# Optimization experiments

Measured on AMD Instinct MI355X. Metric: run time of the kernel, lower is better.

The kernel has to match this reference:

```python
import jax, jax.numpy as jnp
import numpy as np

B, L, D, DEPTH, FF, VOCAB = 2, 2048, 1024, 4, 4096, 32000

def setup_inputs():
    key = jax.random.key(0)
    ks = jax.random.split(key, 16)
    n = lambda k, s, sc: jax.random.normal(k, s, dtype=jnp.float32) * sc
    sw = 0.01 / float(np.sqrt(D))  # xavier_normal with gain 0.01 on square dims
    return dict(
        tokens=jax.random.randint(ks[0], (B, L), 0, VOCAB),
        emb=n(ks[1], (VOCAB, D), 0.02),
        Wz=n(ks[2], (DEPTH, D, D), sw), bz=jnp.zeros((DEPTH, D)),
        Wza=n(ks[3], (DEPTH, D, D), sw), bza=jnp.zeros((DEPTH, D)),
        Wy=n(ks[4], (DEPTH, D, D), sw), by=jnp.zeros((DEPTH, D)),
        Wya=n(ks[5], (DEPTH, D, D), sw), bya=jnp.zeros((DEPTH, D)),
        lc_re=n(ks[6], (DEPTH, D), 1.0), lc_im=n(ks[7], (DEPTH, D), 1.0),
        g_in=jnp.ones((DEPTH, D)), g_sc=jnp.ones((DEPTH, D)), g_ffn=jnp.ones((DEPTH, D)),
        Wf=n(ks[8], (DEPTH, D, FF), 0.02), bf=jnp.zeros((DEPTH, FF)),
        Wfa=n(ks[9], (DEPTH, D, FF), 0.02), bfa=jnp.zeros((DEPTH, FF)),
        Wfo=n(ks[10], (DEPTH, FF, D), 0.02), bfo=jnp.zeros((DEPTH, D)),
        ln_w=jnp.ones((D,)), ln_b=jnp.zeros((D,)),
        Wout=n(ks[11], (D, VOCAB), 0.02), bout=jnp.zeros((VOCAB,)),
    )

def _silu(x):
    return x * jax.nn.sigmoid(x)

def _rms(x, w, eps=1e-6):
    return x * jax.lax.rsqrt(jnp.mean(x * x, axis=-1, keepdims=True) + eps) * w

def reference(tokens, emb, Wz, bz, Wza, bza, Wy, by, Wya, bya, lc_re, lc_im,
              g_in, g_sc, g_ffn, Wf, bf, Wfa, bfa, Wfo, bfo, ln_w, ln_b, Wout, bout):
    Bq, Lq = tokens.shape
    # Embedding with max_norm=1: torch renorms accessed rows to norm <= 1
    e = emb[tokens]
    nrm = jnp.linalg.norm(e, axis=-1, keepdims=True)
    x = e * jnp.minimum(1.0, 1.0 / jnp.maximum(nrm, 1e-7))
    # Decaying phazor kernel (shared across layers; phazor_angle_scale is a fixed buffer)
    angle = jnp.power(0.001, jnp.linspace(0.0, 1.0, D))
    ln_ph = (1e-5 + 1j * angle).astype(jnp.complex64)      # [D]
    t = jnp.arange(Lq, dtype=jnp.float32)
    ph = jnp.exp(t[:, None] * ln_ph[None, :])              # [L, D] complex
    pf = jnp.fft.fft(ph, n=2 * Lq, axis=0)                 # [2L, D]
    decay = jnp.exp(ln_ph)                                 # [D]
    for i in range(DEPTH):
        # --- SConv sublayer (pre-RMSNorm + residual) ---
        xr = x
        xn = _rms(x, g_sc[i])
        z = (xn @ Wz[i] + bz[i]) * _silu(xn @ Wza[i] + bza[i])
        zf = jnp.fft.fft(z.astype(jnp.complex64), n=2 * Lq, axis=1)
        h = jnp.fft.ifft(zf * pf[None], axis=1)[:, :Lq]    # inner-chunk causal decaying conv
        lc = (lc_re[i] + 1j * lc_im[i]).astype(jnp.complex64)
        h = h + lc[None, None, :] * ph[None] * decay[None, None, :]  # cross-chunk state carry
        y = (_rms(h.real, g_in[i]) @ Wy[i] + by[i]) * _silu(xn @ Wya[i] + bya[i])
        x = xr + y
        # --- FFN SwiGLU sublayer (pre-RMSNorm + residual) ---
        xr = x
        xn = _rms(x, g_ffn[i])
        x = xr + ((xn @ Wf[i] + bf[i]) * _silu(xn @ Wfa[i] + bfa[i])) @ Wfo[i] + bfo[i]
    # Final LayerNorm + vocab projection
    mu = jnp.mean(x, axis=-1, keepdims=True)
    var = jnp.mean((x - mu) ** 2, axis=-1, keepdims=True)
    x = (x - mu) * jax.lax.rsqrt(var + 1e-5) * ln_w + ln_b
    return x @ Wout + bout
```

## Files before the change

kernel.cpp:

```cpp
#include <hip/hip_runtime.h>
#include <math.h>

typedef __attribute__((ext_vector_type(8))) short bf16x8;
typedef __attribute__((ext_vector_type(4))) float f32x4;

#define DEVI __device__ __forceinline__

DEVI short f2bf(float f) {
  unsigned u = __builtin_bit_cast(unsigned, f);
  return (short)((u + 0x7fffu + ((u >> 16) & 1u)) >> 16);
}
DEVI float bf2f(short s) {
  unsigned u = ((unsigned)(unsigned short)s) << 16;
  return __builtin_bit_cast(float, u);
}

DEVI float silu_f(float v) { return v / (1.0f + expf(-v)); }

DEVI void async16(const void* g, void* l) {
  __builtin_amdgcn_global_load_lds(
      (const __attribute__((address_space(1))) void*)g,
      (__attribute__((address_space(3))) void*)l, 16, 0, 0);
}

template <int N>
DEVI void waitvm() { asm volatile("s_waitcnt vmcnt(%0)" ::"i"(N) : "memory"); }
DEVI void barrier_mem() { asm volatile("s_barrier" ::: "memory"); }
DEVI void lgkm0_sb() {
  asm volatile("s_waitcnt lgkmcnt(0)" ::: "memory");
  __builtin_amdgcn_sched_barrier(0);
}

template <int NROWT>
DEVI void tile_map(int* bx, int* by) {
  const int nwg = gridDim.x;
  const int lin = blockIdx.x;
  const int q = nwg >> 3;
  const int wgid = (lin & 7) * q + (lin >> 3);
  *by = wgid % NROWT;
  *bx = wgid / NROWT;
}

#define SWZ(r) ((ks ^ (((r) >> 1) & 3)) << 4)

__global__ __launch_bounds__(512, 1) void gemm8_k(const short* __restrict__ A,
                                                  const short* __restrict__ BT,
                                                  const float* __restrict__ bias,
                                                  float* __restrict__ outp,
                                                  int N, int K) {
  __shared__ __align__(16) char lds[4 * 32768];
  int bx, by;
  tile_map<16>(&bx, &by);
  const int row0 = by << 8, col0 = bx << 8;
  const int t = threadIdx.x, w = t >> 6, lane = t & 63;
  const int wm = w >> 2, wn = w & 3;
  const int lr = lane & 15, ks = lane >> 4;
  f32x4 acc[8][4] = {};

  const int sslot = (t & 3) ^ ((t >> 3) & 3);
  const char* gA = (const char*)A + ((size_t)(row0 + (t >> 2)) * K) * 2 + sslot * 16;
  const char* gB = (const char*)BT + ((size_t)(col0 + (t >> 2)) * K) * 2 + sslot * 16;
  const size_t cstep = (size_t)K << 8;
  const int t16 = t << 4;
  const int nkt = K >> 5;

#define SA8(nb, kt)                                                           \
  {                                                                           \
    const size_t co = (size_t)(kt) << 6;                                      \
    async16(gA + co, (nb) + t16);                                             \
    async16(gA + cstep + co, (nb) + 8192 + t16);                              \
  }
#define SB8(nb, kt)                                                           \
  {                                                                           \
    const size_t co = (size_t)(kt) << 6;                                      \
    async16(gB + co, (nb) + 16384 + t16);                                     \
    async16(gB + cstep + co, (nb) + 24576 + t16);                             \
  }
#define RB8()                                                                 \
  _Pragma("unroll") for (int n = 0; n < 4; ++n) {                             \
    const int rb = (wn << 6) + (n << 4) + lr;                                 \
    bfr[n] = *(const bf16x8*)(base + 16384 + rb * 64 + SWZ(rb));              \
  }
#define RA8(mh)                                                               \
  _Pragma("unroll") for (int m = 0; m < 4; ++m) {                             \
    const int r = (wm << 7) + ((mh) << 6) + (m << 4) + lr;                    \
    af[m] = *(const bf16x8*)(base + r * 64 + SWZ(r));                         \
  }
#define MM8(mh)                                                               \
  __builtin_amdgcn_s_setprio(1);                                              \
  _Pragma("unroll") for (int m = 0; m < 4; ++m)                               \
  _Pragma("unroll") for (int n = 0; n < 4; ++n)                               \
      acc[(mh) * 4 + m][n] = __builtin_amdgcn_mfma_f32_16x16x32_bf16(         \
          af[m], bfr[n], acc[(mh) * 4 + m][n], 0, 0, 0);                      \
  __builtin_amdgcn_s_setprio(0);                                              \
  __builtin_amdgcn_sched_barrier(0);

  SA8(lds, 0); SB8(lds, 0);
  SA8(lds + 32768, 1); SB8(lds + 32768, 1);
  SA8(lds + 65536, 2); SB8(lds + 65536, 2);

  for (int kt = 0; kt < nkt; ++kt) {
    const char* base = lds + (kt & 3) * 32768;
    char* nb = lds + ((kt + 3) & 3) * 32768;
    const int rem = nkt - kt;
    bf16x8 af[4], bfr[4];
    if (rem > 2) waitvm<8>();
    else if (rem == 2) waitvm<4>();
    else waitvm<0>();
    barrier_mem();
    if (kt + 3 < nkt) SA8(nb, kt + 3);
    RB8(); RA8(0);
    lgkm0_sb();
    MM8(0);
    barrier_mem();
    if (kt + 3 < nkt) SB8(nb, kt + 3);
    RA8(1);
    lgkm0_sb();
    MM8(1);
  }

  const int orow = row0 + (wm << 7) + (ks << 2);
  const int ocol = col0 + (wn << 6) + lr;
#pragma unroll
  for (int mf = 0; mf < 8; ++mf) {
#pragma unroll
    for (int n = 0; n < 4; ++n) {
      const int c = ocol + (n << 4);
      const float bv = bias[c];
#pragma unroll
      for (int i = 0; i < 4; ++i) {
        const int r = orow + (mf << 4) + i;
        outp[(size_t)r * N + c] = acc[mf][n][i] + bv;
      }
    }
  }
#undef SA8
#undef SB8
#undef RB8
#undef RA8
#undef MM8
}

__global__ __launch_bounds__(512, 1) void dual8_k(const short* __restrict__ A,
                                                  const short* __restrict__ BT1,
                                                  const short* __restrict__ BT2,
                                                  const float* __restrict__ bias1,
                                                  const float* __restrict__ bias2,
                                                  short* __restrict__ outp,
                                                  int N, int K) {
  __shared__ __align__(16) char lds[4 * 32768];
  int bx, by;
  tile_map<16>(&bx, &by);
  const int row0 = by << 8, col0 = bx << 7;
  const int t = threadIdx.x, w = t >> 6, lane = t & 63;
  const int wm = w >> 1, wn = w & 1;
  const int lr = lane & 15, ks = lane >> 4;
  f32x4 acc1[4][4] = {}, acc2[4][4] = {};

  const int sslot = (t & 3) ^ ((t >> 3) & 3);
  const char* gA = (const char*)A + ((size_t)(row0 + (t >> 2)) * K) * 2 + sslot * 16;
  const char* gB1 = (const char*)BT1 + ((size_t)(col0 + (t >> 2)) * K) * 2 + sslot * 16;
  const char* gB2 = (const char*)BT2 + ((size_t)(col0 + (t >> 2)) * K) * 2 + sslot * 16;
  const size_t cstep = (size_t)K << 8;
  const int t16 = t << 4;
  const int nkt = K >> 5;

#define SAD(nb, kt)                                                           \
  {                                                                           \
    const size_t co = (size_t)(kt) << 6;                                      \
    async16(gA + co, (nb) + t16);                                             \
    async16(gA + cstep + co, (nb) + 8192 + t16);                              \
  }
#define SB1D(nb, kt) async16(gB1 + ((size_t)(kt) << 6), (nb) + 16384 + t16)
#define SB2D(nb, kt) async16(gB2 + ((size_t)(kt) << 6), (nb) + 24576 + t16)

  SAD(lds, 0); SB1D(lds, 0); SB2D(lds, 0);
  SAD(lds + 32768, 1); SB1D(lds + 32768, 1); SB2D(lds + 32768, 1);
  SAD(lds + 65536, 2); SB1D(lds + 65536, 2); SB2D(lds + 65536, 2);

  for (int kt = 0; kt < nkt; ++kt) {
    const char* base = lds + (kt & 3) * 32768;
    char* nb = lds + ((kt + 3) & 3) * 32768;
    const int rem = nkt - kt;
    bf16x8 af[4], bfr[4];
    if (rem > 2) waitvm<8>();
    else if (rem == 2) waitvm<4>();
    else waitvm<0>();
    barrier_mem();
    if (kt + 3 < nkt) SAD(nb, kt + 3);
#pragma unroll
    for (int n = 0; n < 4; ++n) {
      const int rb = (wn << 6) + (n << 4) + lr;
      bfr[n] = *(const bf16x8*)(base + 16384 + rb * 64 + SWZ(rb));
    }
#pragma unroll
    for (int m = 0; m < 4; ++m) {
      const int r = (wm << 6) + (m << 4) + lr;
      af[m] = *(const bf16x8*)(base + r * 64 + SWZ(r));
    }
    lgkm0_sb();
    __builtin_amdgcn_s_setprio(1);
#pragma unroll
    for (int m = 0; m < 4; ++m)
#pragma unroll
      for (int n = 0; n < 4; ++n)
        acc1[m][n] = __builtin_amdgcn_mfma_f32_16x16x32_bf16(af[m], bfr[n], acc1[m][n], 0, 0, 0);
    __builtin_amdgcn_s_setprio(0);
    __builtin_amdgcn_sched_barrier(0);
    barrier_mem();
    if (kt + 3 < nkt) { SB1D(nb, kt + 3); SB2D(nb, kt + 3); }
#pragma unroll
    for (int n = 0; n < 4; ++n) {
      const int rb = (wn << 6) + (n << 4) + lr;
      bfr[n] = *(const bf16x8*)(base + 24576 + rb * 64 + SWZ(rb));
    }
    lgkm0_sb();
    __builtin_amdgcn_s_setprio(1);
#pragma unroll
    for (int m = 0; m < 4; ++m)
#pragma unroll
      for (int n = 0; n < 4; ++n)
        acc2[m][n] = __builtin_amdgcn_mfma_f32_16x16x32_bf16(af[m], bfr[n], acc2[m][n], 0, 0, 0);
    __builtin_amdgcn_s_setprio(0);
    __builtin_amdgcn_sched_barrier(0);
  }

  const int orow = row0 + (wm << 6) + (ks << 2);
  const int ocol = col0 + (wn << 6) + lr;
#pragma unroll
  for (int m = 0; m < 4; ++m) {
#pragma unroll
    for (int n = 0; n < 4; ++n) {
      const int c = ocol + (n << 4);
      const float bv1 = bias1[c], bv2 = bias2[c];
#pragma unroll
      for (int i = 0; i < 4; ++i) {
        const int r = orow + (m << 4) + i;
        outp[(size_t)r * N + c] = f2bf((acc1[m][n][i] + bv1) * silu_f(acc2[m][n][i] + bv2));
      }
    }
  }
#undef SAD
#undef SB1D
#undef SB2D
}

__global__ __launch_bounds__(256, 2) void triple_k(const short* __restrict__ A,
                                                   const short* __restrict__ BT1,
                                                   const short* __restrict__ BT2,
                                                   const short* __restrict__ BT3,
                                                   const float* __restrict__ b1,
                                                   const float* __restrict__ b2,
                                                   const float* __restrict__ b3,
                                                   short* __restrict__ zout,
                                                   short* __restrict__ yaout,
                                                   int N, int K) {
  constexpr int PBB = 28672;
  __shared__ __align__(16) char lds[2 * PBB];
  int bx, by;
  tile_map<64>(&bx, &by);
  const int row0 = by << 6, col0 = bx << 7;
  const int t = threadIdx.x, w = t >> 6, lane = t & 63;
  const int wr = w >> 1, wc = w & 1;
  const int lr = lane & 15, ks = lane >> 4;
  f32x4 acc1[2][4] = {}, acc2[2][4] = {}, acc3[2][4] = {};

  const int sslot = (t & 3) ^ ((t >> 3) & 3);
  const char* gA = (const char*)A + ((size_t)(row0 + (t >> 2)) * K) * 2 + sslot * 16;
  const size_t brow = ((size_t)(col0 + (t >> 2)) * K) * 2 + sslot * 16;
  const char* gB1 = (const char*)BT1 + brow;
  const char* gB2 = (const char*)BT2 + brow;
  const char* gB3 = (const char*)BT3 + brow;
  const size_t cstep = (size_t)K * 128;
  const int t16 = t << 4;
  const int nkt = K >> 5;

#define STA(nb, kt) async16(gA + (size_t)(kt) * 64, (nb) + t16)
#define STB(nb, kt, gp, off)                                                  \
  {                                                                           \
    const size_t co = (size_t)(kt) * 64;                                      \
    async16((gp) + co, (nb) + (off) + t16);                                   \
    async16((gp) + cstep + co, (nb) + (off) + 4096 + t16);                    \
  }

  { char* nb = lds; STA(nb, 0); STB(nb, 0, gB1, 4096); STB(nb, 0, gB2, 12288); STB(nb, 0, gB3, 20480); }

  for (int kt = 0; kt < nkt; ++kt) {
    const int ktn = kt + 1;
    const char* base = lds + (kt & 1) * PBB;
    char* nb = lds + (ktn & 1) * PBB;
    bf16x8 af[2], bfr[4];
    waitvm<4>();
    barrier_mem();
    if (ktn < nkt) { STA(nb, ktn); STB(nb, ktn, gB1, 4096); }
#pragma unroll
    for (int m = 0; m < 2; ++m) {
      const int r = (wr << 5) + (m << 4) + lr;
      af[m] = *(const bf16x8*)(base + r * 64 + SWZ(r));
    }
#pragma unroll
    for (int n = 0; n < 4; ++n) {
      const int rb = (wc << 6) + (n << 4) + lr;
      bfr[n] = *(const bf16x8*)(base + 4096 + rb * 64 + SWZ(rb));
    }
    lgkm0_sb();
    __builtin_amdgcn_s_setprio(1);
#pragma unroll
    for (int m = 0; m < 2; ++m)
#pragma unroll
      for (int n = 0; n < 4; ++n)
        acc1[m][n] = __builtin_amdgcn_mfma_f32_16x16x32_bf16(af[m], bfr[n], acc1[m][n], 0, 0, 0);
    __builtin_amdgcn_s_setprio(0);
    __builtin_amdgcn_sched_barrier(0);
    if (ktn < nkt) waitvm<5>();
    else waitvm<2>();
    barrier_mem();
    if (ktn < nkt) STB(nb, ktn, gB2, 12288);
#pragma unroll
    for (int n = 0; n < 4; ++n) {
      const int rb = (wc << 6) + (n << 4) + lr;
      bfr[n] = *(const bf16x8*)(base + 12288 + rb * 64 + SWZ(rb));
    }
    lgkm0_sb();
    __builtin_amdgcn_s_setprio(1);
#pragma unroll
    for (int m = 0; m < 2; ++m)
#pragma unroll
      for (int n = 0; n < 4; ++n)
        acc2[m][n] = __builtin_amdgcn_mfma_f32_16x16x32_bf16(af[m], bfr[n], acc2[m][n], 0, 0, 0);
    __builtin_amdgcn_s_setprio(0);
    __builtin_amdgcn_sched_barrier(0);
    if (ktn < nkt) waitvm<5>();
    else waitvm<0>();
    barrier_mem();
    if (ktn < nkt) STB(nb, ktn, gB3, 20480);
#pragma unroll
    for (int n = 0; n < 4; ++n) {
      const int rb = (wc << 6) + (n << 4) + lr;
      bfr[n] = *(const bf16x8*)(base + 20480 + rb * 64 + SWZ(rb));
    }
    lgkm0_sb();
    __builtin_amdgcn_s_setprio(1);
#pragma unroll
    for (int m = 0; m < 2; ++m)
#pragma unroll
      for (int n = 0; n < 4; ++n)
        acc3[m][n] = __builtin_amdgcn_mfma_f32_16x16x32_bf16(af[m], bfr[n], acc3[m][n], 0, 0, 0);
    __builtin_amdgcn_s_setprio(0);
    __builtin_amdgcn_sched_barrier(0);
  }

  const int orow = row0 + (wr << 5) + (ks << 2);
  const int ocol = col0 + (wc << 6) + lr;
#pragma unroll
  for (int m = 0; m < 2; ++m) {
#pragma unroll
    for (int n = 0; n < 4; ++n) {
      const int c = ocol + (n << 4);
      const float bv1 = b1[c], bv2 = b2[c], bv3 = b3[c];
#pragma unroll
      for (int i = 0; i < 4; ++i) {
        const int r = orow + (m << 4) + i;
        const size_t idx = (size_t)r * N + c;
        zout[idx] = f2bf((acc1[m][n][i] + bv1) * silu_f(acc2[m][n][i] + bv2));
        yaout[idx] = f2bf(acc3[m][n][i] + bv3);
      }
    }
  }
#undef STA
#undef STB
}

template <int MODE, int BM, int BN, int WM, int WN, int NBUF>
__global__ __launch_bounds__(256, 2) void gemm_k(const short* __restrict__ A,
                                                 const short* __restrict__ BT,
                                                 const float* __restrict__ bias,
                                                 const short* __restrict__ aux,
                                                 void* __restrict__ outp,
                                                 int N, int K) {
  constexpr int MF = WM / 16, NF = WN / 16;
  constexpr int NWN = BN / WN;
  constexpr int PBB = (BM + BN) * 64;
  constexpr int DEPTH = NBUF - 1;
  constexpr int L = (BM + BN) / 64;
  static_assert((BM / WM) * (BN / WN) == 4, "4 waves");
  __shared__ __align__(16) char lds[NBUF * PBB];
  int bx, by;
  tile_map<4096 / BM>(&bx, &by);
  const int row0 = by * BM, col0 = bx * BN;
  const int t = threadIdx.x, w = t >> 6, lane = t & 63;
  const int wr = w / NWN, wc = w % NWN;
  f32x4 acc[MF][NF] = {};

  const int sslot = (t & 3) ^ ((t >> 3) & 3);
  const char* gA0 = (const char*)A + ((size_t)(row0 + (t >> 2)) * K) * 2 + sslot * 16;
  const char* gB0 = (const char*)BT + ((size_t)(col0 + (t >> 2)) * K) * 2 + sslot * 16;
  const size_t ccstep = (size_t)K * 128;
  const int wb = w << 10;
  const int lr = lane & 15, ks = lane >> 4;

  const int NIT = K >> 5;
  auto stage = [&](int buf, int it) {
    char* dst = lds + buf * PBB;
    const size_t io = (size_t)it * 64;
#pragma unroll
    for (int cc = 0; cc < BM / 64; ++cc)
      async16(gA0 + io + cc * ccstep, dst + cc * 4096 + wb);
#pragma unroll
    for (int cc = 0; cc < BN / 64; ++cc)
      async16(gB0 + io + cc * ccstep, dst + BM * 64 + cc * 4096 + wb);
  };

#pragma unroll
  for (int pit = 0; pit < DEPTH; ++pit) stage(pit, pit);

  for (int it = 0; it < NIT; ++it) {
    const int rem = NIT - it;
    if (rem >= DEPTH + 1) waitvm<L * (DEPTH - 1)>();
    else if (rem >= 2) waitvm<L>();
    else waitvm<0>();
    barrier_mem();
    if (it + DEPTH < NIT) stage((it + DEPTH) % NBUF, it + DEPTH);
    const char* base = lds + (it % NBUF) * PBB;
    bf16x8 af[MF], bfr[NF];
#pragma unroll
    for (int m = 0; m < MF; ++m) {
      const int r = wr * WM + m * 16 + lr;
      af[m] = *(const bf16x8*)(base + r * 64 + SWZ(r));
    }
#pragma unroll
    for (int n = 0; n < NF; ++n) {
      const int r = wc * WN + n * 16 + lr;
      bfr[n] = *(const bf16x8*)(base + BM * 64 + r * 64 + SWZ(r));
    }
    lgkm0_sb();
    __builtin_amdgcn_s_setprio(1);
#pragma unroll
    for (int m = 0; m < MF; ++m)
#pragma unroll
      for (int n = 0; n < NF; ++n)
        acc[m][n] = __builtin_amdgcn_mfma_f32_16x16x32_bf16(af[m], bfr[n], acc[m][n], 0, 0, 0);
    __builtin_amdgcn_s_setprio(0);
    __builtin_amdgcn_sched_barrier(0);
  }

  const int orow = row0 + wr * WM + (ks << 2);
  const int ocol = col0 + wc * WN + lr;
#pragma unroll
  for (int m = 0; m < MF; ++m) {
#pragma unroll
    for (int n = 0; n < NF; ++n) {
      const int c = ocol + (n << 4);
      const float bv = bias[c];
#pragma unroll
      for (int i = 0; i < 4; ++i) {
        const int r = orow + (m << 4) + i;
        const size_t idx = (size_t)r * N + c;
        float v = acc[m][n][i] + bv;
        if (MODE == 0) ((float*)outp)[idx] = v;
        else if (MODE == 3) ((float*)outp)[idx] += v * silu_f(bf2f(aux[idx]));
        else ((float*)outp)[idx] += v;
      }
    }
  }
}

__global__ __launch_bounds__(256) void transp_k(const float* __restrict__ W,
                                                short* __restrict__ WT,
                                                int R, int C) {
  __shared__ float tile[32][33];
  const size_t moff = (size_t)blockIdx.z * R * C;
  const float* Wp = W + moff;
  short* Tp = WT + moff;
  const int c0 = blockIdx.x << 5, r0 = blockIdx.y << 5;
  const int tx = threadIdx.x, ty = threadIdx.y;
#pragma unroll
  for (int i = 0; i < 4; ++i)
    tile[ty + 8 * i][tx] = Wp[(size_t)(r0 + ty + 8 * i) * C + (c0 + tx)];
  __syncthreads();
#pragma unroll
  for (int i = 0; i < 4; ++i)
    Tp[(size_t)(c0 + ty + 8 * i) * R + (r0 + tx)] = f2bf(tile[tx][ty + 8 * i]);
}

__global__ __launch_bounds__(256) void embed_k(const int* __restrict__ tok,
                                               const float* __restrict__ emb,
                                               float* __restrict__ x) {
  const int row = blockIdx.x, t = threadIdx.x, w = t >> 6, lane = t & 63;
  const int token = tok[row];
  float4 v = ((const float4*)(emb + (size_t)token * 1024))[t];
  float ss = v.x * v.x + v.y * v.y + v.z * v.z + v.w * v.w;
#pragma unroll
  for (int off = 32; off; off >>= 1) ss += __shfl_xor(ss, off, 64);
  __shared__ float red[4];
  if (lane == 0) red[w] = ss;
  __syncthreads();
  const float nrm = sqrtf(red[0] + red[1] + red[2] + red[3]);
  const float sc = fminf(1.0f, 1.0f / fmaxf(nrm, 1e-7f));
  v.x *= sc; v.y *= sc; v.z *= sc; v.w *= sc;
  ((float4*)(x + (size_t)row * 1024))[t] = v;
}

template <int BF>
__global__ __launch_bounds__(256) void rms_k(const void* __restrict__ xin,
                                             const float* __restrict__ g,
                                             short* __restrict__ o) {
  const int row = blockIdx.x, t = threadIdx.x, w = t >> 6, lane = t & 63;
  float v0, v1, v2, v3;
  if (BF) {
    short4 s = ((const short4*)((const short*)xin + (size_t)row * 1024))[t];
    v0 = bf2f(s.x); v1 = bf2f(s.y); v2 = bf2f(s.z); v3 = bf2f(s.w);
  } else {
    float4 v = ((const float4*)((const float*)xin + (size_t)row * 1024))[t];
    v0 = v.x; v1 = v.y; v2 = v.z; v3 = v.w;
  }
  float ss = v0 * v0 + v1 * v1 + v2 * v2 + v3 * v3;
#pragma unroll
  for (int off = 32; off; off >>= 1) ss += __shfl_xor(ss, off, 64);
  __shared__ float red[4];
  if (lane == 0) red[w] = ss;
  __syncthreads();
  const float sc = rsqrtf((red[0] + red[1] + red[2] + red[3]) * (1.0f / 1024.0f) + 1e-6f);
  float4 gv = ((const float4*)g)[t];
  short4 ov = make_short4(f2bf(v0 * sc * gv.x), f2bf(v1 * sc * gv.y),
                          f2bf(v2 * sc * gv.z), f2bf(v3 * sc * gv.w));
  *(short4*)(o + (size_t)row * 1024 + 4 * t) = ov;
}

__global__ __launch_bounds__(256) void ln_k(const float* __restrict__ x,
                                            const float* __restrict__ lw,
                                            const float* __restrict__ lb,
                                            short* __restrict__ o) {
  const int row = blockIdx.x, t = threadIdx.x, w = t >> 6, lane = t & 63;
  float4 v = ((const float4*)(x + (size_t)row * 1024))[t];
  float s1 = v.x + v.y + v.z + v.w;
  float s2 = v.x * v.x + v.y * v.y + v.z * v.z + v.w * v.w;
#pragma unroll
  for (int off = 32; off; off >>= 1) {
    s1 += __shfl_xor(s1, off, 64);
    s2 += __shfl_xor(s2, off, 64);
  }
  __shared__ float red[8];
  if (lane == 0) { red[w] = s1; red[4 + w] = s2; }
  __syncthreads();
  const float mu = (red[0] + red[1] + red[2] + red[3]) * (1.0f / 1024.0f);
  const float ex2 = (red[4] + red[5] + red[6] + red[7]) * (1.0f / 1024.0f);
  const float rs = rsqrtf(ex2 - mu * mu + 1e-5f);
  float4 wv = ((const float4*)lw)[t];
  float4 bv = ((const float4*)lb)[t];
  short4 ov = make_short4(f2bf((v.x - mu) * rs * wv.x + bv.x),
                          f2bf((v.y - mu) * rs * wv.y + bv.y),
                          f2bf((v.z - mu) * rs * wv.z + bv.z),
                          f2bf((v.w - mu) * rs * wv.w + bv.w));
  *(short4*)(o + (size_t)row * 1024 + 4 * t) = ov;
}

DEVI void decay_of(int d, float* dr, float* di) {
  const float ang = powf(1e-3f, (float)d * (1.0f / 1023.0f));
  float sn, cs;
  sincosf(ang, &sn, &cs);
  const float mag = expf(1e-5f);
  *dr = mag * cs; *di = mag * sn;
}

__global__ __launch_bounds__(256) void s1_k(const short* __restrict__ z,
                                            float* __restrict__ Er, float* __restrict__ Ei) {
  const int d = (blockIdx.x << 8) + threadIdx.x;
  const int c = blockIdx.y, b = blockIdx.z;
  float dr, di;
  decay_of(d, &dr, &di);
  const short* zp = z + ((size_t)(b * 2048 + c * 64) << 10) + d;
  float sr = 0.0f, si = 0.0f;
  for (int k = 0; k < 64; ++k) {
    float zv = bf2f(zp[(size_t)k << 10]);
    float nr = dr * sr - di * si + zv;
    si = dr * si + di * sr;
    sr = nr;
  }
  const int idx = ((b << 5) + c) * 1024 + d;
  Er[idx] = sr; Ei[idx] = si;
}

__global__ __launch_bounds__(256) void s3_k(const short* __restrict__ z,
                                            const float* __restrict__ Er,
                                            const float* __restrict__ Ei,
                                            const float* __restrict__ lcre,
                                            const float* __restrict__ lcim,
                                            short* __restrict__ h) {
  const int d = (blockIdx.x << 8) + threadIdx.x;
  const int c = blockIdx.y, b = blockIdx.z;
  float dr, di;
  decay_of(d, &dr, &di);
  float ar = dr, ai = di;
#pragma unroll
  for (int q = 0; q < 6; ++q) { float nr = ar * ar - ai * ai; ai = 2.0f * ar * ai; ar = nr; }
  float sr = 0.0f, si = 0.0f;
  for (int cc = 0; cc < c; ++cc) {
    const int eidx = ((b << 5) + cc) * 1024 + d;
    const float er = Er[eidx], ei = Ei[eidx];
    const float nr = ar * sr - ai * si + er;
    si = ar * si + ai * sr + ei;
    sr = nr;
  }
  float wr = 1.0f, wi = 0.0f, br = ar, bi = ai;
  int e = c;
  while (e) {
    if (e & 1) { float nr = wr * br - wi * bi; wi = wr * bi + wi * br; wr = nr; }
    float nb = br * br - bi * bi; bi = 2.0f * br * bi; br = nb;
    e >>= 1;
  }
  { float nr = wr * dr - wi * di; wi = wr * di + wi * dr; wr = nr; }
  const float lr_ = lcre[d], li_ = lcim[d];
  const size_t base = ((size_t)(b * 2048 + c * 64) << 10) + d;
  for (int k = 0; k < 64; ++k) {
    const float zv = bf2f(z[base + ((size_t)k << 10)]);
    const float nr = dr * sr - di * si + zv;
    si = dr * si + di * sr;
    sr = nr;
    h[base + ((size_t)k << 10)] = f2bf(sr + lr_ * wr - li_ * wi);
    const float nw = wr * dr - wi * di;
    wi = wr * di + wi * dr;
    wr = nw;
  }
}

extern "C" void kernel_launch(void* const* d_in, const int* in_sizes, int n_in,
                              void* d_out, int out_size, void* d_ws, size_t ws_size,
                              hipStream_t stream) {
  const int* tokens = (const int*)d_in[0];
  const float* emb = (const float*)d_in[1];
  const float* Wz = (const float*)d_in[2];
  const float* bz = (const float*)d_in[3];
  const float* Wza = (const float*)d_in[4];
  const float* bza = (const float*)d_in[5];
  const float* Wy = (const float*)d_in[6];
  const float* by = (const float*)d_in[7];
  const float* Wya = (const float*)d_in[8];
  const float* bya = (const float*)d_in[9];
  const float* lc_re = (const float*)d_in[10];
  const float* lc_im = (const float*)d_in[11];
  const float* g_in = (const float*)d_in[12];
  const float* g_sc = (const float*)d_in[13];
  const float* g_ffn = (const float*)d_in[14];
  const float* Wf = (const float*)d_in[15];
  const float* bf = (const float*)d_in[16];
  const float* Wfa = (const float*)d_in[17];
  const float* bfa = (const float*)d_in[18];
  const float* Wfo = (const float*)d_in[19];
  const float* bfo = (const float*)d_in[20];
  const float* ln_w = (const float*)d_in[21];
  const float* ln_b = (const float*)d_in[22];
  const float* Wout = (const float*)d_in[23];
  const float* bout = (const float*)d_in[24];

  char* p = (char*)d_ws;
  float* xb = (float*)p;   p += (size_t)4096 * 1024 * 4;
  short* zb = (short*)p;   p += (size_t)4096 * 1024 * 2;
  short* hb = (short*)p;   p += (size_t)4096 * 1024 * 2;
  short* yab = (short*)p;  p += (size_t)4096 * 1024 * 2;
  float* Er = (float*)p;   p += (size_t)2 * 32 * 1024 * 4;
  float* Ei = (float*)p;   p += (size_t)2 * 32 * 1024 * 4;
  short* xnb = (short*)p;  p += (size_t)4096 * 1024 * 2;
  short* hnb = (short*)p;  p += (size_t)4096 * 1024 * 2;
  short* gb = (short*)p;   p += (size_t)4096 * 4096 * 2;
  short* WzT = (short*)p;  p += (size_t)4 * 1024 * 1024 * 2;
  short* WzaT = (short*)p; p += (size_t)4 * 1024 * 1024 * 2;
  short* WyT = (short*)p;  p += (size_t)4 * 1024 * 1024 * 2;
  short* WyaT = (short*)p; p += (size_t)4 * 1024 * 1024 * 2;
  short* WfT = (short*)p;  p += (size_t)4 * 1024 * 4096 * 2;
  short* WfaT = (short*)p; p += (size_t)4 * 1024 * 4096 * 2;
  short* WfoT = (short*)p; p += (size_t)4 * 1024 * 4096 * 2;
  short* WoutT = (short*)p; p += (size_t)32000 * 1024 * 2;

  const dim3 tb(32, 8);
  transp_k<<<dim3(32, 32, 4), tb, 0, stream>>>(Wz, WzT, 1024, 1024);
  transp_k<<<dim3(32, 32, 4), tb, 0, stream>>>(Wza, WzaT, 1024, 1024);
  transp_k<<<dim3(32, 32, 4), tb, 0, stream>>>(Wy, WyT, 1024, 1024);
  transp_k<<<dim3(32, 32, 4), tb, 0, stream>>>(Wya, WyaT, 1024, 1024);
  transp_k<<<dim3(128, 32, 4), tb, 0, stream>>>(Wf, WfT, 1024, 4096);
  transp_k<<<dim3(128, 32, 4), tb, 0, stream>>>(Wfa, WfaT, 1024, 4096);
  transp_k<<<dim3(32, 128, 4), tb, 0, stream>>>(Wfo, WfoT, 4096, 1024);
  transp_k<<<dim3(1000, 32, 1), tb, 0, stream>>>(Wout, WoutT, 1024, 32000);

  embed_k<<<4096, 256, 0, stream>>>(tokens, emb, xb);

  for (int i = 0; i < 4; ++i) {
    const size_t dd = (size_t)i * 1024 * 1024;
    const size_t dv = (size_t)i * 1024;
    const size_t dw = (size_t)i * 1024 * 4096;
    const size_t df = (size_t)i * 4096;
    rms_k<0><<<4096, 256, 0, stream>>>(xb, g_sc + dv, xnb);
    triple_k<<<512, 256, 0, stream>>>(xnb, WzT + dd, WzaT + dd, WyaT + dd,
                                      bz + dv, bza + dv, bya + dv, zb, yab, 1024, 1024);
    s1_k<<<dim3(4, 32, 2), 256, 0, stream>>>(zb, Er, Ei);
    s3_k<<<dim3(4, 32, 2), 256, 0, stream>>>(zb, Er, Ei, lc_re + dv, lc_im + dv, hb);
    rms_k<1><<<4096, 256, 0, stream>>>(hb, g_in + dv, hnb);
    gemm_k<3, 64, 128, 32, 64, 3><<<512, 256, 0, stream>>>(
        hnb, WyT + dd, by + dv, yab, xb, 1024, 1024);
    rms_k<0><<<4096, 256, 0, stream>>>(xb, g_ffn + dv, xnb);
    dual8_k<<<512, 512, 0, stream>>>(xnb, WfT + dw, WfaT + dw, bf + df, bfa + df,
                                     gb, 4096, 1024);
    gemm_k<4, 64, 128, 32, 64, 4><<<512, 256, 0, stream>>>(
        gb, WfoT + dw, bfo + dv, nullptr, xb, 1024, 4096);
  }

  ln_k<<<4096, 256, 0, stream>>>(xb, ln_w, ln_b, xnb);
  gemm8_k<<<2000, 512, 0, stream>>>(xnb, WoutT, bout, (float*)d_out, 32000, 1024);

  (void)in_sizes; (void)n_in; (void)out_size; (void)ws_size;
}
```

Measured before the change: 1.561 ms.

## Shrink vocab and FFN-dual GEMM tiles for higher occupancy with 3-stage pipeline

The vocab projection kernel goes from 256x256 tiles at one block per CU to 256x128 tiles with a 3-buffer, 2-ahead pipeline and launch bounds allowing four blocks. The FFN dual GEMM moves from 512-thread 256x128 tiles to 256-thread 128x128 tiles, interleaving both MFMA chains in one phase per k-step. The aim is more resident waves to hide latency and fewer barriers per k-step. The cost is lower operand reuse per tile, so more global and LDS traffic, and a shallower prefetch depth.

```diff
diff --git a/kernel.cpp b/kernel.cpp
--- a/kernel.cpp
+++ b/kernel.cpp
@@ -43,19 +43,19 @@
 
 #define SWZ(r) ((ks ^ (((r) >> 1) & 3)) << 4)
 
-__global__ __launch_bounds__(512, 1) void gemm8_k(const short* __restrict__ A,
-                                                  const short* __restrict__ BT,
-                                                  const float* __restrict__ bias,
-                                                  float* __restrict__ outp,
-                                                  int N, int K) {
-  __shared__ __align__(16) char lds[4 * 32768];
+__global__ __launch_bounds__(512, 4) void voc_k(const short* __restrict__ A,
+                                                const short* __restrict__ BT,
+                                                const float* __restrict__ bias,
+                                                float* __restrict__ outp,
+                                                int N, int K) {
+  __shared__ __align__(16) char lds[3 * 24576];
   int bx, by;
   tile_map<16>(&bx, &by);
-  const int row0 = by << 8, col0 = bx << 8;
+  const int row0 = by << 8, col0 = bx << 7;
   const int t = threadIdx.x, w = t >> 6, lane = t & 63;
-  const int wm = w >> 2, wn = w & 3;
+  const int wm = w >> 1, wn = w & 1;
   const int lr = lane & 15, ks = lane >> 4;
-  f32x4 acc[8][4] = {};
+  f32x4 acc[4][4] = {};
 
   const int sslot = (t & 3) ^ ((t >> 3) & 3);
   const char* gA = (const char*)A + ((size_t)(row0 + (t >> 2)) * K) * 2 + sslot * 16;
@@ -64,94 +64,75 @@
   const int t16 = t << 4;
   const int nkt = K >> 5;
 
-#define SA8(nb, kt)                                                           \
+#define SV(nb, kt)                                                            \
   {                                                                           \
     const size_t co = (size_t)(kt) << 6;                                      \
     async16(gA + co, (nb) + t16);                                             \
     async16(gA + cstep + co, (nb) + 8192 + t16);                              \
-  }
-#define SB8(nb, kt)                                                           \
-  {                                                                           \
-    const size_t co = (size_t)(kt) << 6;                                      \
     async16(gB + co, (nb) + 16384 + t16);                                     \
-    async16(gB + cstep + co, (nb) + 24576 + t16);                             \
-  }
-#define RB8()                                                                 \
-  _Pragma("unroll") for (int n = 0; n < 4; ++n) {                             \
-    const int rb = (wn << 6) + (n << 4) + lr;                                 \
-    bfr[n] = *(const bf16x8*)(base + 16384 + rb * 64 + SWZ(rb));              \
-  }
-#define RA8(mh)                                                               \
-  _Pragma("unroll") for (int m = 0; m < 4; ++m) {                             \
-    const int r = (wm << 7) + ((mh) << 6) + (m << 4) + lr;                    \
-    af[m] = *(const bf16x8*)(base + r * 64 + SWZ(r));                         \
-  }
-#define MM8(mh)                                                               \
-  __builtin_amdgcn_s_setprio(1);                                              \
-  _Pragma("unroll") for (int m = 0; m < 4; ++m)                               \
-  _Pragma("unroll") for (int n = 0; n < 4; ++n)                               \
-      acc[(mh) * 4 + m][n] = __builtin_amdgcn_mfma_f32_16x16x32_bf16(         \
-          af[m], bfr[n], acc[(mh) * 4 + m][n], 0, 0, 0);                      \
-  __builtin_amdgcn_s_setprio(0);                                              \
-  __builtin_amdgcn_sched_barrier(0);
-
-  SA8(lds, 0); SB8(lds, 0);
-  SA8(lds + 32768, 1); SB8(lds + 32768, 1);
-  SA8(lds + 65536, 2); SB8(lds + 65536, 2);
+  }
+
+  SV(lds, 0);
+  SV(lds + 24576, 1);
 
   for (int kt = 0; kt < nkt; ++kt) {
-    const char* base = lds + (kt & 3) * 32768;
-    char* nb = lds + ((kt + 3) & 3) * 32768;
-    const int rem = nkt - kt;
-    bf16x8 af[4], bfr[4];
-    if (rem > 2) waitvm<8>();
-    else if (rem == 2) waitvm<4>();
+    const char* base = lds + (kt % 3) * 24576;
+    char* nb = lds + ((kt + 2) % 3) * 24576;
+    if (kt + 1 < nkt) waitvm<3>();
     else waitvm<0>();
     barrier_mem();
-    if (kt + 3 < nkt) SA8(nb, kt + 3);
-    RB8(); RA8(0);
+    if (kt + 2 < nkt) SV(nb, kt + 2);
+    bf16x8 af[4], bfr[4];
+#pragma unroll
+    for (int m = 0; m < 4; ++m) {
+      const int r = (wm << 6) + (m << 4) + lr;
+      af[m] = *(const bf16x8*)(base + r * 64 + SWZ(r));
+    }
+#pragma unroll
+    for (int n = 0; n < 4; ++n) {
+      const int rb = (wn << 6) + (n << 4) + lr;
+      bfr[n] = *(const bf16x8*)(base + 16384 + rb * 64 + SWZ(rb));
+    }
     lgkm0_sb();
-    MM8(0);
-    barrier_mem();
-    if (kt + 3 < nkt) SB8(nb, kt + 3);
-    RA8(1);
-    lgkm0_sb();
-    MM8(1);
-  }
-
-  const int orow = row0 + (wm << 7) + (ks << 2);
+    __builtin_amdgcn_s_setprio(1);
+#pragma unroll
+    for (int m = 0; m < 4; ++m)
+#pragma unroll
+      for (int n = 0; n < 4; ++n)
+        acc[m][n] = __builtin_amdgcn_mfma_f32_16x16x32_bf16(af[m], bfr[n], acc[m][n], 0, 0, 0);
+    __builtin_amdgcn_s_setprio(0);
+    __builtin_amdgcn_sched_barrier(0);
+  }
+
+  const int orow = row0 + (wm << 6) + (ks << 2);
   const int ocol = col0 + (wn << 6) + lr;
 #pragma unroll
-  for (int mf = 0; mf < 8; ++mf) {
+  for (int m = 0; m < 4; ++m) {
 #pragma unroll
     for (int n = 0; n < 4; ++n) {
       const int c = ocol + (n << 4);
       const float bv = bias[c];
 #pragma unroll
       for (int i = 0; i < 4; ++i) {
-        const int r = orow + (mf << 4) + i;
-        outp[(size_t)r * N + c] = acc[mf][n][i] + bv;
+        const int r = orow + (m << 4) + i;
+        outp[(size_t)r * N + c] = acc[m][n][i] + bv;
       }
     }
   }
-#undef SA8
-#undef SB8
-#undef RB8
-#undef RA8
-#undef MM8
-}
-
-__global__ __launch_bounds__(512, 1) void dual8_k(const short* __restrict__ A,
-                                                  const short* __restrict__ BT1,
-                                                  const short* __restrict__ BT2,
-                                                  const float* __restrict__ bias1,
-                                                  const float* __restrict__ bias2,
-                                                  short* __restrict__ outp,
-                                                  int N, int K) {
-  __shared__ __align__(16) char lds[4 * 32768];
+#undef SV
+}
+
+__global__ __launch_bounds__(256, 2) void dual_k(const short* __restrict__ A,
+                                                 const short* __restrict__ BT1,
+                                                 const short* __restrict__ BT2,
+                                                 const float* __restrict__ bias1,
+                                                 const float* __restrict__ bias2,
+                                                 short* __restrict__ outp,
+                                                 int N, int K) {
+  __shared__ __align__(16) char lds[3 * 24576];
   int bx, by;
-  tile_map<16>(&bx, &by);
-  const int row0 = by << 8, col0 = bx << 7;
+  tile_map<32>(&bx, &by);
+  const int row0 = by << 7, col0 = bx << 7;
   const int t = threadIdx.x, w = t >> 6, lane = t & 63;
   const int wm = w >> 1, wn = w & 1;
   const int lr = lane & 15, ks = lane >> 4;
@@ -161,66 +142,52 @@
   const char* gA = (const char*)A + ((size_t)(row0 + (t >> 2)) * K) * 2 + sslot * 16;
   const char* gB1 = (const char*)BT1 + ((size_t)(col0 + (t >> 2)) * K) * 2 + sslot * 16;
   const char* gB2 = (const char*)BT2 + ((size_t)(col0 + (t >> 2)) * K) * 2 + sslot * 16;
-  const size_t cstep = (size_t)K << 8;
+  const size_t cstep = (size_t)K << 7;
   const int t16 = t << 4;
   const int nkt = K >> 5;
 
-#define SAD(nb, kt)                                                           \
+#define SD(nb, kt)                                                            \
   {                                                                           \
     const size_t co = (size_t)(kt) << 6;                                      \
     async16(gA + co, (nb) + t16);                                             \
-    async16(gA + cstep + co, (nb) + 8192 + t16);                              \
-  }
-#define SB1D(nb, kt) async16(gB1 + ((size_t)(kt) << 6), (nb) + 16384 + t16)
-#define SB2D(nb, kt) async16(gB2 + ((size_t)(kt) << 6), (nb) + 24576 + t16)
-
-  SAD(lds, 0); SB1D(lds, 0); SB2D(lds, 0);
-  SAD(lds + 32768, 1); SB1D(lds + 32768, 1); SB2D(lds + 32768, 1);
-  SAD(lds + 65536, 2); SB1D(lds + 65536, 2); SB2D(lds + 65536, 2);
+    async16(gA + cstep + co, (nb) + 4096 + t16);                              \
+    async16(gB1 + co, (nb) + 8192 + t16);                                     \
+    async16(gB1 + cstep + co, (nb) + 12288 + t16);                            \
+    async16(gB2 + co, (nb) + 16384 + t16);                                    \
+    async16(gB2 + cstep + co, (nb) + 20480 + t16);                            \
+  }
+
+  SD(lds, 0);
+  SD(lds + 24576, 1);
 
   for (int kt = 0; kt < nkt; ++kt) {
-    const char* base = lds + (kt & 3) * 32768;
-    char* nb = lds + ((kt + 3) & 3) * 32768;
-    const int rem = nkt - kt;
-    bf16x8 af[4], bfr[4];
-    if (rem > 2) waitvm<8>();
-    else if (rem == 2) waitvm<4>();
+    const char* base = lds + (kt % 3) * 24576;
+    char* nb = lds + ((kt + 2) % 3) * 24576;
+    if (kt + 1 < nkt) waitvm<6>();
     else waitvm<0>();
     barrier_mem();
-    if (kt + 3 < nkt) SAD(nb, kt + 3);
-#pragma unroll
-    for (int n = 0; n < 4; ++n) {
-      const int rb = (wn << 6) + (n << 4) + lr;
-      bfr[n] = *(const bf16x8*)(base + 16384 + rb * 64 + SWZ(rb));
-    }
+    if (kt + 2 < nkt) SD(nb, kt + 2);
+    bf16x8 af[4], b1r[4], b2r[4];
 #pragma unroll
     for (int m = 0; m < 4; ++m) {
       const int r = (wm << 6) + (m << 4) + lr;
       af[m] = *(const bf16x8*)(base + r * 64 + SWZ(r));
     }
+#pragma unroll
+    for (int n = 0; n < 4; ++n) {
+      const int rb = (wn << 6) + (n << 4) + lr;
+      b1r[n] = *(const bf16x8*)(base + 8192 + rb * 64 + SWZ(rb));
+      b2r[n] = *(const bf16x8*)(base + 16384 + rb * 64 + SWZ(rb));
+    }
     lgkm0_sb();
     __builtin_amdgcn_s_setprio(1);
 #pragma unroll
     for (int m = 0; m < 4; ++m)
 #pragma unroll
-      for (int n = 0; n < 4; ++n)
-        acc1[m][n] = __builtin_amdgcn_mfma_f32_16x16x32_bf16(af[m], bfr[n], acc1[m][n], 0, 0, 0);
-    __builtin_amdgcn_s_setprio(0);
-    __builtin_amdgcn_sched_barrier(0);
-    barrier_mem();
-    if (kt + 3 < nkt) { SB1D(nb, kt + 3); SB2D(nb, kt + 3); }
-#pragma unroll
-    for (int n = 0; n < 4; ++n) {
-      const int rb = (wn << 6) + (n << 4) + lr;
-      bfr[n] = *(const bf16x8*)(base + 24576 + rb * 64 + SWZ(rb));
-    }
-    lgkm0_sb();
-    __builtin_amdgcn_s_setprio(1);
-#pragma unroll
-    for (int m = 0; m < 4; ++m)
-#pragma unroll
-      for (int n = 0; n < 4; ++n)
-        acc2[m][n] = __builtin_amdgcn_mfma_f32_16x16x32_bf16(af[m], bfr[n], acc2[m][n], 0, 0, 0);
+      for (int n = 0; n < 4; ++n) {
+        acc1[m][n] = __builtin_amdgcn_mfma_f32_16x16x32_bf16(af[m], b1r[n], acc1[m][n], 0, 0, 0);
+        acc2[m][n] = __builtin_amdgcn_mfma_f32_16x16x32_bf16(af[m], b2r[n], acc2[m][n], 0, 0, 0);
+      }
     __builtin_amdgcn_s_setprio(0);
     __builtin_amdgcn_sched_barrier(0);
   }
@@ -240,9 +207,7 @@
       }
     }
   }
-#undef SAD
-#undef SB1D
-#undef SB2D
+#undef SD
 }
 
 __global__ __launch_bounds__(256, 2) void triple_k(const short* __restrict__ A,
@@ -698,14 +663,14 @@
     gemm_k<3, 64, 128, 32, 64, 3><<<512, 256, 0, stream>>>(
         hnb, WyT + dd, by + dv, yab, xb, 1024, 1024);
     rms_k<0><<<4096, 256, 0, stream>>>(xb, g_ffn + dv, xnb);
-    dual8_k<<<512, 512, 0, stream>>>(xnb, WfT + dw, WfaT + dw, bf + df, bfa + df,
+    dual_k<<<1024, 256, 0, stream>>>(xnb, WfT + dw, WfaT + dw, bf + df, bfa + df,
                                      gb, 4096, 1024);
     gemm_k<4, 64, 128, 32, 64, 4><<<512, 256, 0, stream>>>(
         gb, WfoT + dw, bfo + dv, nullptr, xb, 1024, 4096);
   }
 
   ln_k<<<4096, 256, 0, stream>>>(xb, ln_w, ln_b, xnb);
-  gemm8_k<<<2000, 512, 0, stream>>>(xnb, WoutT, bout, (float*)d_out, 32000, 1024);
+  voc_k<<<4000, 512, 0, stream>>>(xnb, WoutT, bout, (float*)d_out, 32000, 1024);
 
   (void)in_sizes; (void)n_in; (void)out_size; (void)ws_size;
 }
```

Result: slower. 1.592 ms (+2.0%).
